# Optimization experiments

Measured on AMD Instinct MI355X. Metric: run time of the kernel, lower is better.

Reference implementation:

```python
import jax, jax.numpy as jnp
import numpy as np

L, H, P = 131072, 128, 128
STEP_RESCALE = 1.0
CONJ_SYM = True


def setup_inputs() -> dict:
    key = jax.random.key(0)
    ks = jax.random.split(key, 9)
    x = jax.random.normal(ks[0], (L, H), jnp.float32)
    # stable SSM: real parts of Lambda must be negative so |dA| < 1
    A_real_log = -(0.5 + jax.random.uniform(ks[1], (P,), jnp.float32))
    A_imag = 3.0 * jax.random.normal(ks[2], (P,), jnp.float32)
    B_re = jax.random.normal(ks[3], (P, H), jnp.float32) / np.sqrt(H)
    B_im = jax.random.normal(ks[4], (P, H), jnp.float32) / np.sqrt(H)
    C_re = jax.random.normal(ks[5], (H, P), jnp.float32) / np.sqrt(P)
    C_im = jax.random.normal(ks[6], (H, P), jnp.float32) / np.sqrt(P)
    D = jax.random.normal(ks[7], (H,), jnp.float32)
    # softplus(inv_dt) small -> small timestep dt
    inv_dt = jax.random.normal(ks[8], (P,), jnp.float32) - 4.0
    return {"x": x, "A_real_log": A_real_log, "A_imag": A_imag,
            "B_re": B_re, "B_im": B_im, "C_re": C_re, "C_im": C_im,
            "D": D, "inv_dt": inv_dt}


def reference(x, A_real_log, A_imag, B_re, B_im, C_re, C_im, D, inv_dt):
    # A = Lambda (diagonal complex state matrix), shape (P,)
    A = A_real_log + 1j * A_imag
    dt = STEP_RESCALE * jax.nn.softplus(inv_dt)            # (P,)
    # bilinear (Tustin) discretization
    BL = 1.0 / (1.0 - 0.5 * dt * A)                        # (P,)
    dA = BL * (1.0 + 0.5 * dt * A)                         # (P,)
    B = B_re + 1j * B_im                                   # (P,H)
    dB = (BL * dt)[:, None] * B                            # (P,H)
    # input projection into state space: (L,P) complex
    Bu = jnp.einsum('lh,ph->lp', x + 0j, dB)
    # linear recurrence h_k = dA * h_{k-1} + Bu_k via parallel associative scan
    A_elems = jnp.broadcast_to(dA[None, :], Bu.shape)
    def binop(q1, q2):
        a1, b1 = q1
        a2, b2 = q2
        return a1 * a2, a2 * b1 + b2
    _, hs = jax.lax.associative_scan(binop, (A_elems, Bu), axis=0)  # (L,P)
    C = C_re + 1j * C_im                                   # (H,P)
    y = jnp.einsum('lp,hp->lh', hs, C).real                # (L,H)
    if CONJ_SYM:
        y = 2.0 * y
    return y + x * D[None, :]
```

## Files before the change

### kernel.cpp

```cpp
#include <hip/hip_runtime.h>

#define L_LEN 131072
#define H_DIM 128
#define P_DIM 128
#define SEG 32
#define NSEG (L_LEN / SEG)
#define ROWS 64
#define NBLK (L_LEN / ROWS)

typedef unsigned int uint32;
typedef unsigned short u16;
typedef short bf16x8 __attribute__((ext_vector_type(8)));
typedef float f32x4 __attribute__((ext_vector_type(4)));

constexpr size_t OFF_HL  = 0;
constexpr size_t N_HLF   = (size_t)L_LEN * 256 / 2;
constexpr size_t OFF_DA  = OFF_HL + N_HLF;
constexpr size_t OFF_POW = OFF_DA + 256;
constexpr size_t OFF_E   = OFF_POW + 32 * 256;
constexpr size_t OFF_HIN = OFF_E + (size_t)NSEG * 256;
constexpr size_t OFF_W1F = OFF_HIN + (size_t)NSEG * 256;
constexpr size_t OFF_W2F = OFF_W1F + 32768;

__device__ __forceinline__ u16 f2bf(float v) {
    uint32 u = __builtin_bit_cast(uint32, v);
    uint32 r = u + 0x7FFFu + ((u >> 16) & 1u);
    return (u16)(r >> 16);
}
__device__ __forceinline__ float bf2f(u16 h) {
    uint32 u = ((uint32)h) << 16;
    return __builtin_bit_cast(float, u);
}
__device__ __forceinline__ uint32 cvtpk(float lo, float hi) {
    uint32 r;
    asm("v_cvt_pk_bf16_f32 %0, %1, %2" : "=v"(r) : "v"(lo), "v"(hi));
    return r;
}
__device__ __forceinline__ float2 cfma(float2 a, float2 h, float2 c) {
    float2 r;
    r.x = fmaf(a.x, h.x, fmaf(-a.y, h.y, c.x));
    r.y = fmaf(a.x, h.y, fmaf(a.y, h.x, c.y));
    return r;
}
__device__ __forceinline__ float2 cmul(float2 a, float2 b) {
    return make_float2(fmaf(a.x, b.x, -a.y * b.y), fmaf(a.x, b.y, a.y * b.x));
}
__device__ __forceinline__ float2 unpk(uint32 w) {
    return make_float2(bf2f((u16)(w & 0xffffu)), bf2f((u16)(w >> 16)));
}
__device__ __forceinline__ bf16x8 fixup(uint4 hl, f32x4 d0, f32x4 d1, f32x4 h0, f32x4 h1) {
    float2 c0 = cfma(make_float2(d0[0], d0[1]), make_float2(h0[0], h0[1]), unpk(hl.x));
    float2 c1 = cfma(make_float2(d0[2], d0[3]), make_float2(h0[2], h0[3]), unpk(hl.y));
    float2 c2 = cfma(make_float2(d1[0], d1[1]), make_float2(h1[0], h1[1]), unpk(hl.z));
    float2 c3 = cfma(make_float2(d1[2], d1[3]), make_float2(h1[2], h1[3]), unpk(hl.w));
    union { uint32 u[4]; bf16x8 v; } r;
    r.u[0] = cvtpk(c0.x, c0.y); r.u[1] = cvtpk(c1.x, c1.y);
    r.u[2] = cvtpk(c2.x, c2.y); r.u[3] = cvtpk(c3.x, c3.y);
    return r.v;
}

__global__ void k0(const float* __restrict__ Arl, const float* __restrict__ Ai,
                   const float* __restrict__ invdt,
                   const float* __restrict__ Bre, const float* __restrict__ Bim,
                   const float* __restrict__ Cre, const float* __restrict__ Cim,
                   float* __restrict__ dA, float* __restrict__ dApow,
                   u16* __restrict__ W1F, u16* __restrict__ W2F) {
    int tid = blockIdx.x * 256 + threadIdx.x;
    int lane = tid & 63;
    int fb = (tid >> 6) & 63;
    int ar = lane & 15, aq = lane >> 4;
    ushort4 hiA, hiB, loA, loB;
    u16* dst;
    if (tid < 4096) {
        int kt = fb >> 4, cf = fb & 15;
        int q = cf * 16 + ar;
        int p = q >> 1, c = q & 1;
        int h0 = kt * 32 + aq * 8;
        float idt = invdt[p];
        float dt = (idt > 20.f) ? idt : log1pf(expf(idt));
        float arl = Arl[p], aii = Ai[p];
        float zr = 0.5f * dt * arl, zi = 0.5f * dt * aii;
        float drr = 1.f - zr, dii = -zi;
        float inv = 1.f / (drr * drr + dii * dii);
        float blr = drr * inv, bli = -dii * inv;
        float2 s = make_float2(blr * dt, bli * dt);
        u16 hh[8], ll[8];
        #pragma unroll
        for (int j = 0; j < 8; ++j) {
            float br = Bre[p * H_DIM + h0 + j], bi = Bim[p * H_DIM + h0 + j];
            float re = fmaf(s.x, br, -s.y * bi);
            float im = fmaf(s.x, bi,  s.y * br);
            float v = c ? im : re;
            u16 h = f2bf(v); hh[j] = h; ll[j] = f2bf(v - bf2f(h));
        }
        hiA = make_ushort4(hh[0], hh[1], hh[2], hh[3]);
        hiB = make_ushort4(hh[4], hh[5], hh[6], hh[7]);
        loA = make_ushort4(ll[0], ll[1], ll[2], ll[3]);
        loB = make_ushort4(ll[4], ll[5], ll[6], ll[7]);
        dst = W1F + fb * 1024 + lane * 8;
    } else {
        int kk = fb >> 3, cf = fb & 7;
        int h = cf * 16 + ar;
        int q0 = kk * 32 + aq * 8;
        u16 hh[8], ll[8];
        #pragma unroll
        for (int j = 0; j < 8; ++j) {
            int q = q0 + j; int p = q >> 1;
            float v = (q & 1) ? (-2.f * Cim[h * P_DIM + p]) : (2.f * Cre[h * P_DIM + p]);
            u16 hv = f2bf(v); hh[j] = hv; ll[j] = f2bf(v - bf2f(hv));
        }
        hiA = make_ushort4(hh[0], hh[1], hh[2], hh[3]);
        hiB = make_ushort4(hh[4], hh[5], hh[6], hh[7]);
        loA = make_ushort4(ll[0], ll[1], ll[2], ll[3]);
        loB = make_ushort4(ll[4], ll[5], ll[6], ll[7]);
        dst = W2F + fb * 1024 + lane * 8;
    }
    *(ushort4*)(dst)       = hiA;
    *(ushort4*)(dst + 4)   = hiB;
    *(ushort4*)(dst + 512) = loA;
    *(ushort4*)(dst + 516) = loB;

    if (blockIdx.x == 0 && threadIdx.x < 128) {
        int p = threadIdx.x;
        float idt = invdt[p];
        float dt = (idt > 20.f) ? idt : log1pf(expf(idt));
        float arl = Arl[p], aii = Ai[p];
        float zr = 0.5f * dt * arl, zi = 0.5f * dt * aii;
        float drr = 1.f - zr, dii = -zi;
        float inv = 1.f / (drr * drr + dii * dii);
        float blr = drr * inv, bli = -dii * inv;
        float nr = 1.f + zr, ni = zi;
        float2 a = make_float2(fmaf(blr, nr, -bli * ni), fmaf(blr, ni, bli * nr));
        dA[2 * p] = a.x; dA[2 * p + 1] = a.y;
        float2 pw = a;
        for (int i = 0; i < SEG; ++i) {
            dApow[((size_t)i * P_DIM + p) * 2]     = pw.x;
            dApow[((size_t)i * P_DIM + p) * 2 + 1] = pw.y;
            pw = cmul(pw, a);
        }
    }
}

__global__ __launch_bounds__(256) void k1(const float* __restrict__ x,
                                          const u16* __restrict__ W1F,
                                          const float* __restrict__ dA,
                                          u16* __restrict__ HL,
                                          float* __restrict__ E) {
    __shared__ __align__(16) char smem[32768];
    u16* As_hi = (u16*)smem;
    u16* SB    = (u16*)smem;
    int t = threadIdx.x, lane = t & 63, wid = t >> 6;
    size_t l0 = (size_t)blockIdx.x * ROWS;
    int ar = lane & 15, aq = lane >> 4, ak = aq * 8;

    bf16x8 bhp[4][4];
    #pragma unroll
    for (int kt = 0; kt < 4; ++kt)
        #pragma unroll
        for (int nf = 0; nf < 4; ++nf)
            bhp[kt][nf] = *(const bf16x8*)(W1F + (size_t)(kt * 16 + wid * 4 + nf) * 1024 + lane * 8);

    float4 xv[8];
    #pragma unroll
    for (int j = 0; j < 8; ++j) {
        int f = j * 256 + t; int row = f >> 5, c4 = f & 31;
        xv[j] = *(const float4*)(x + (l0 + row) * H_DIM + c4 * 4);
    }
    #pragma unroll
    for (int j = 0; j < 8; ++j) {
        int f = j * 256 + t; int row = f >> 5, c4 = f & 31;
        uint2 wv;
        wv.x = cvtpk(xv[j].x, xv[j].y);
        wv.y = cvtpk(xv[j].z, xv[j].w);
        *(uint2*)&As_hi[row * 136 + c4 * 4] = wv;
    }
    __syncthreads();

    f32x4 acc[4][4];
    #pragma unroll
    for (int a = 0; a < 4; ++a)
        #pragma unroll
        for (int b = 0; b < 4; ++b) acc[a][b] = (f32x4)0.f;

    #pragma unroll
    for (int kt = 0; kt < 4; ++kt) {
        bf16x8 ah[4];
        #pragma unroll
        for (int mf = 0; mf < 4; ++mf) {
            int row = mf * 16 + ar;
            ah[mf] = *(const bf16x8*)&As_hi[row * 136 + kt * 32 + ak];
        }
        #pragma unroll
        for (int nf = 0; nf < 4; ++nf)
            #pragma unroll
            for (int mf = 0; mf < 4; ++mf)
                acc[mf][nf] = __builtin_amdgcn_mfma_f32_16x16x32_bf16(ah[mf], bhp[kt][nf], acc[mf][nf], 0, 0, 0);
    }
    __syncthreads();

    int sr = aq * 4;
    #pragma unroll
    for (int mf = 0; mf < 4; ++mf)
        #pragma unroll
        for (int nf = 0; nf < 4; ++nf) {
            int col = wid * 64 + nf * 16 + ar;
            uint32 w01 = cvtpk(acc[mf][nf][0], acc[mf][nf][1]);
            uint32 w23 = cvtpk(acc[mf][nf][2], acc[mf][nf][3]);
            int r0 = mf * 16 + sr;
            SB[(r0 + 0) * 256 + (((col >> 3) ^ ((r0 + 0) & 7)) << 3) + (col & 7)] = (u16)w01;
            SB[(r0 + 1) * 256 + (((col >> 3) ^ ((r0 + 1) & 7)) << 3) + (col & 7)] = (u16)(w01 >> 16);
            SB[(r0 + 2) * 256 + (((col >> 3) ^ ((r0 + 2) & 7)) << 3) + (col & 7)] = (u16)w23;
            SB[(r0 + 3) * 256 + (((col >> 3) ^ ((r0 + 3) & 7)) << 3) + (col & 7)] = (u16)(w23 >> 16);
        }
    __syncthreads();

    {
        int s = t >> 7, p = t & 127;
        float2 a = ((const float2*)dA)[p];
        uint32 buf[SEG];
        #pragma unroll
        for (int i = 0; i < SEG; ++i) {
            int row = s * 32 + i;
            buf[i] = *(const uint32*)&SB[row * 256 + (((p >> 2) ^ (row & 7)) << 3) + (p & 3) * 2];
        }
        float2 h = make_float2(0.f, 0.f);
        #pragma unroll
        for (int i = 0; i < SEG; ++i) {
            h = cfma(a, h, unpk(buf[i]));
            buf[i] = cvtpk(h.x, h.y);
        }
        #pragma unroll
        for (int i = 0; i < SEG; ++i) {
            int row = s * 32 + i;
            *(uint32*)&SB[row * 256 + (((p >> 2) ^ (row & 7)) << 3) + (p & 3) * 2] = buf[i];
        }
        ((float2*)E)[((size_t)blockIdx.x * 2 + s) * P_DIM + p] = h;
    }
    __syncthreads();

    #pragma unroll
    for (int j = 0; j < 8; ++j) {
        int f = j * 256 + t; int row = f >> 5, blk = f & 31;
        uint4 v = *(const uint4*)&SB[row * 256 + ((blk ^ (row & 7)) << 3)];
        *(uint4*)(HL + (l0 + row) * 256 + blk * 8) = v;
    }
}

__global__ __launch_bounds__(256) void k3(const float* __restrict__ E,
                                          const float* __restrict__ dA,
                                          float* __restrict__ Hin) {
    __shared__ float4 wagg[4];
    int m = blockIdx.x, t = threadIdx.x;
    int lane = t & 63, w = t >> 6;
    float2 aS = ((const float2*)dA)[m];
    #pragma unroll
    for (int i = 0; i < 5; ++i) aS = cmul(aS, aS);
    const float2* e = (const float2*)E;
    float2 ebuf[16];
    #pragma unroll
    for (int i = 0; i < 16; ++i) ebuf[i] = e[(size_t)(t * 16 + i) * P_DIM + m];
    float2 Bv = ebuf[0];
    #pragma unroll
    for (int i = 1; i < 16; ++i) Bv = cfma(aS, Bv, ebuf[i]);
    float2 Av = aS;
    #pragma unroll
    for (int i = 0; i < 4; ++i) Av = cmul(Av, Av);

    #pragma unroll
    for (int d = 1; d < 64; d <<= 1) {
        float uAx = __shfl_up(Av.x, (unsigned)d, 64);
        float uAy = __shfl_up(Av.y, (unsigned)d, 64);
        float uBx = __shfl_up(Bv.x, (unsigned)d, 64);
        float uBy = __shfl_up(Bv.y, (unsigned)d, 64);
        if (lane >= d) {
            float2 uA = make_float2(uAx, uAy), uB = make_float2(uBx, uBy);
            Bv = cfma(Av, uB, Bv);
            Av = cmul(uA, Av);
        }
    }
    if (lane == 63) wagg[w] = make_float4(Av.x, Av.y, Bv.x, Bv.y);
    __syncthreads();
    float2 Pb = make_float2(0.f, 0.f);
    for (int i = 0; i < w; ++i) {
        float4 u = wagg[i];
        float2 Wa = make_float2(u.x, u.y), Wb = make_float2(u.z, u.w);
        Pb = cfma(Wa, Pb, Wb);
    }
    float eAx = __shfl_up(Av.x, 1u, 64), eAy = __shfl_up(Av.y, 1u, 64);
    float eBx = __shfl_up(Bv.x, 1u, 64), eBy = __shfl_up(Bv.y, 1u, 64);
    float2 eA = make_float2(eAx, eAy), eB = make_float2(eBx, eBy);
    if (lane == 0) { eA = make_float2(1.f, 0.f); eB = make_float2(0.f, 0.f); }
    float2 pre = cfma(eA, Pb, eB);
    float2* hin = (float2*)Hin;
    #pragma unroll
    for (int i = 0; i < 16; ++i) {
        hin[(size_t)(t * 16 + i) * P_DIM + m] = pre;
        pre = cfma(aS, pre, ebuf[i]);
    }
}

__global__ __launch_bounds__(256) void k4(const float* __restrict__ x,
                                          const u16* __restrict__ HL,
                                          const u16* __restrict__ W2F,
                                          const float* __restrict__ dApow,
                                          const float* __restrict__ Hin,
                                          const float* __restrict__ Dv,
                                          float* __restrict__ y) {
    __shared__ __align__(16) char smem[34816];
    u16*   SB   = (u16*)smem;
    float* HinS = (float*)(smem + 32768);
    float* SBF  = (float*)smem;
    int t = threadIdx.x, lane = t & 63, wid = t >> 6;
    size_t l0 = (size_t)blockIdx.x * ROWS;

    bf16x8 bhp[8][2];
    #pragma unroll
    for (int kk = 0; kk < 8; ++kk)
        #pragma unroll
        for (int nf = 0; nf < 2; ++nf)
            bhp[kk][nf] = *(const bf16x8*)(W2F + (size_t)(kk * 8 + wid * 2 + nf) * 1024 + lane * 8);

    ((float2*)HinS)[t] = ((const float2*)Hin)[(size_t)blockIdx.x * 2 * P_DIM + t];
    __syncthreads();

    uint4 va[8];
    #pragma unroll
    for (int j = 0; j < 8; ++j) {
        int f = j * 256 + t; int row = f >> 5, blk = f & 31;
        va[j] = *(const uint4*)(HL + (l0 + row) * 256 + blk * 8);
    }
    f32x4 da[8][2];
    #pragma unroll
    for (int j = 0; j < 8; ++j) {
        int f = j * 256 + t; int row = f >> 5, blk = f & 31;
        const float* dp = dApow + (size_t)(row & 31) * 256 + blk * 8;
        da[j][0] = *(const f32x4*)dp;
        da[j][1] = *(const f32x4*)(dp + 4);
    }
    #pragma unroll
    for (int j = 0; j < 8; ++j) {
        int f = j * 256 + t; int row = f >> 5, blk = f & 31;
        int sg = row >> 5;
        f32x4 h0 = *(const f32x4*)&HinS[sg * 256 + blk * 8];
        f32x4 h1 = *(const f32x4*)&HinS[sg * 256 + blk * 8 + 4];
        bf16x8 o = fixup(va[j], da[j][0], da[j][1], h0, h1);
        *(bf16x8*)&SB[row * 256 + ((blk ^ (row & 7)) << 3)] = o;
    }
    __syncthreads();

    f32x4 acc[4][2];
    #pragma unroll
    for (int a = 0; a < 4; ++a)
        #pragma unroll
        for (int b = 0; b < 2; ++b) acc[a][b] = (f32x4)0.f;
    int ar = lane & 15, aq = lane >> 4;
    #pragma unroll
    for (int kk = 0; kk < 8; ++kk) {
        bf16x8 af[4];
        #pragma unroll
        for (int mf = 0; mf < 4; ++mf) {
            int row = mf * 16 + ar;
            int blk = kk * 4 + aq;
            af[mf] = *(const bf16x8*)&SB[row * 256 + ((blk ^ (row & 7)) << 3)];
        }
        #pragma unroll
        for (int nf = 0; nf < 2; ++nf)
            #pragma unroll
            for (int mf = 0; mf < 4; ++mf)
                acc[mf][nf] = __builtin_amdgcn_mfma_f32_16x16x32_bf16(af[mf], bhp[kk][nf], acc[mf][nf], 0, 0, 0);
    }
    __syncthreads();

    int sr = aq * 4;
    #pragma unroll
    for (int mf = 0; mf < 4; ++mf)
        #pragma unroll
        for (int nf = 0; nf < 2; ++nf)
            #pragma unroll
            for (int r = 0; r < 4; ++r) {
                int row = mf * 16 + sr + r;
                int col = wid * 32 + nf * 16 + ar;
                SBF[row * 130 + col] = acc[mf][nf][r];
            }
    __syncthreads();

    int c4 = t & 31;
    float4 dv = *(const float4*)(Dv + c4 * 4);
    #pragma unroll
    for (int j = 0; j < 8; ++j) {
        int row = j * 8 + (t >> 5);
        float4 sv = *(float4*)&SBF[row * 130 + c4 * 4];
        float4 xv = *(const float4*)(x + (l0 + row) * H_DIM + c4 * 4);
        float4 out;
        out.x = fmaf(xv.x, dv.x, sv.x);
        out.y = fmaf(xv.y, dv.y, sv.y);
        out.z = fmaf(xv.z, dv.z, sv.z);
        out.w = fmaf(xv.w, dv.w, sv.w);
        *(float4*)(y + (l0 + row) * H_DIM + c4 * 4) = out;
    }
}

extern "C" void kernel_launch(void* const* d_in, const int* in_sizes, int n_in,
                              void* d_out, int out_size, void* d_ws, size_t ws_size,
                              hipStream_t stream) {
    const float* x     = (const float*)d_in[0];
    const float* Arl   = (const float*)d_in[1];
    const float* Ai    = (const float*)d_in[2];
    const float* Bre   = (const float*)d_in[3];
    const float* Bim   = (const float*)d_in[4];
    const float* Cre   = (const float*)d_in[5];
    const float* Cim   = (const float*)d_in[6];
    const float* Dv    = (const float*)d_in[7];
    const float* invdt = (const float*)d_in[8];
    float* y  = (float*)d_out;
    float* ws = (float*)d_ws;

    u16* hl  = (u16*)(ws + OFF_HL);
    u16* w1f = (u16*)(ws + OFF_W1F);
    u16* w2f = (u16*)(ws + OFF_W2F);

    k0<<<32, 256, 0, stream>>>(Arl, Ai, invdt, Bre, Bim, Cre, Cim,
                               ws + OFF_DA, ws + OFF_POW, w1f, w2f);
    k1<<<NBLK, 256, 0, stream>>>(x, w1f, ws + OFF_DA, hl, ws + OFF_E);
    k3<<<128, 256, 0, stream>>>(ws + OFF_E, ws + OFF_DA, ws + OFF_HIN);
    k4<<<NBLK, 256, 0, stream>>>(x, hl, w2f, ws + OFF_POW,
                                 ws + OFF_HIN, Dv, y);
}
```

Measured before the change: 86.43 us.

## Recompute input projection in final kernel instead of storing local scan states

The first pass now computes only each segment's end state and no longer writes the full bf16 local hidden states (L x 256 values) to global memory. The final kernel recomputes x·dB with MFMA, runs the recurrence from the propagated carry-in state, and then applies the C projection. The dA power table and the fixup step are removed. This drops a large global write and read of the intermediate state in exchange for doing the first GEMM twice and running a serial 32-step scan in the last kernel.

```diff
diff --git a/kernel.cpp b/kernel.cpp
--- a/kernel.cpp
+++ b/kernel.cpp
@@ -13,11 +13,8 @@
 typedef short bf16x8 __attribute__((ext_vector_type(8)));
 typedef float f32x4 __attribute__((ext_vector_type(4)));
 
-constexpr size_t OFF_HL  = 0;
-constexpr size_t N_HLF   = (size_t)L_LEN * 256 / 2;
-constexpr size_t OFF_DA  = OFF_HL + N_HLF;
-constexpr size_t OFF_POW = OFF_DA + 256;
-constexpr size_t OFF_E   = OFF_POW + 32 * 256;
+constexpr size_t OFF_DA  = 0;
+constexpr size_t OFF_E   = OFF_DA + 256;
 constexpr size_t OFF_HIN = OFF_E + (size_t)NSEG * 256;
 constexpr size_t OFF_W1F = OFF_HIN + (size_t)NSEG * 256;
 constexpr size_t OFF_W2F = OFF_W1F + 32768;
@@ -48,22 +45,12 @@
 __device__ __forceinline__ float2 unpk(uint32 w) {
     return make_float2(bf2f((u16)(w & 0xffffu)), bf2f((u16)(w >> 16)));
 }
-__device__ __forceinline__ bf16x8 fixup(uint4 hl, f32x4 d0, f32x4 d1, f32x4 h0, f32x4 h1) {
-    float2 c0 = cfma(make_float2(d0[0], d0[1]), make_float2(h0[0], h0[1]), unpk(hl.x));
-    float2 c1 = cfma(make_float2(d0[2], d0[3]), make_float2(h0[2], h0[3]), unpk(hl.y));
-    float2 c2 = cfma(make_float2(d1[0], d1[1]), make_float2(h1[0], h1[1]), unpk(hl.z));
-    float2 c3 = cfma(make_float2(d1[2], d1[3]), make_float2(h1[2], h1[3]), unpk(hl.w));
-    union { uint32 u[4]; bf16x8 v; } r;
-    r.u[0] = cvtpk(c0.x, c0.y); r.u[1] = cvtpk(c1.x, c1.y);
-    r.u[2] = cvtpk(c2.x, c2.y); r.u[3] = cvtpk(c3.x, c3.y);
-    return r.v;
-}
 
 __global__ void k0(const float* __restrict__ Arl, const float* __restrict__ Ai,
                    const float* __restrict__ invdt,
                    const float* __restrict__ Bre, const float* __restrict__ Bim,
                    const float* __restrict__ Cre, const float* __restrict__ Cim,
-                   float* __restrict__ dA, float* __restrict__ dApow,
+                   float* __restrict__ dA,
                    u16* __restrict__ W1F, u16* __restrict__ W2F) {
     int tid = blockIdx.x * 256 + threadIdx.x;
     int lane = tid & 63;
@@ -130,21 +117,14 @@
         float inv = 1.f / (drr * drr + dii * dii);
         float blr = drr * inv, bli = -dii * inv;
         float nr = 1.f + zr, ni = zi;
-        float2 a = make_float2(fmaf(blr, nr, -bli * ni), fmaf(blr, ni, bli * nr));
-        dA[2 * p] = a.x; dA[2 * p + 1] = a.y;
-        float2 pw = a;
-        for (int i = 0; i < SEG; ++i) {
-            dApow[((size_t)i * P_DIM + p) * 2]     = pw.x;
-            dApow[((size_t)i * P_DIM + p) * 2 + 1] = pw.y;
-            pw = cmul(pw, a);
-        }
+        dA[2 * p]     = fmaf(blr, nr, -bli * ni);
+        dA[2 * p + 1] = fmaf(blr, ni,  bli * nr);
     }
 }
 
 __global__ __launch_bounds__(256) void k1(const float* __restrict__ x,
                                           const u16* __restrict__ W1F,
                                           const float* __restrict__ dA,
-                                          u16* __restrict__ HL,
                                           float* __restrict__ E) {
     __shared__ __align__(16) char smem[32768];
     u16* As_hi = (u16*)smem;
@@ -181,15 +161,12 @@
     for (int a = 0; a < 4; ++a)
         #pragma unroll
         for (int b = 0; b < 4; ++b) acc[a][b] = (f32x4)0.f;
-
     #pragma unroll
     for (int kt = 0; kt < 4; ++kt) {
         bf16x8 ah[4];
         #pragma unroll
-        for (int mf = 0; mf < 4; ++mf) {
-            int row = mf * 16 + ar;
-            ah[mf] = *(const bf16x8*)&As_hi[row * 136 + kt * 32 + ak];
-        }
+        for (int mf = 0; mf < 4; ++mf)
+            ah[mf] = *(const bf16x8*)&As_hi[(mf * 16 + ar) * 136 + kt * 32 + ak];
         #pragma unroll
         for (int nf = 0; nf < 4; ++nf)
             #pragma unroll
@@ -223,26 +200,10 @@
             int row = s * 32 + i;
             buf[i] = *(const uint32*)&SB[row * 256 + (((p >> 2) ^ (row & 7)) << 3) + (p & 3) * 2];
         }
-        float2 h = make_float2(0.f, 0.f);
-        #pragma unroll
-        for (int i = 0; i < SEG; ++i) {
-            h = cfma(a, h, unpk(buf[i]));
-            buf[i] = cvtpk(h.x, h.y);
-        }
-        #pragma unroll
-        for (int i = 0; i < SEG; ++i) {
-            int row = s * 32 + i;
-            *(uint32*)&SB[row * 256 + (((p >> 2) ^ (row & 7)) << 3) + (p & 3) * 2] = buf[i];
-        }
-        ((float2*)E)[((size_t)blockIdx.x * 2 + s) * P_DIM + p] = h;
-    }
-    __syncthreads();
-
-    #pragma unroll
-    for (int j = 0; j < 8; ++j) {
-        int f = j * 256 + t; int row = f >> 5, blk = f & 31;
-        uint4 v = *(const uint4*)&SB[row * 256 + ((blk ^ (row & 7)) << 3)];
-        *(uint4*)(HL + (l0 + row) * 256 + blk * 8) = v;
+        float2 e = make_float2(0.f, 0.f);
+        #pragma unroll
+        for (int i = 0; i < SEG; ++i) e = cfma(a, e, unpk(buf[i]));
+        ((float2*)E)[((size_t)blockIdx.x * 2 + s) * P_DIM + p] = e;
     }
 }
 
@@ -300,60 +261,114 @@
 }
 
 __global__ __launch_bounds__(256) void k4(const float* __restrict__ x,
-                                          const u16* __restrict__ HL,
+                                          const u16* __restrict__ W1F,
                                           const u16* __restrict__ W2F,
-                                          const float* __restrict__ dApow,
+                                          const float* __restrict__ dA,
                                           const float* __restrict__ Hin,
                                           const float* __restrict__ Dv,
                                           float* __restrict__ y) {
-    __shared__ __align__(16) char smem[34816];
-    u16*   SB   = (u16*)smem;
-    float* HinS = (float*)(smem + 32768);
-    float* SBF  = (float*)smem;
+    __shared__ __align__(16) char smem[33280];
+    u16*   As_hi = (u16*)smem;
+    u16*   SB    = (u16*)smem;
+    float* SBF   = (float*)smem;
     int t = threadIdx.x, lane = t & 63, wid = t >> 6;
     size_t l0 = (size_t)blockIdx.x * ROWS;
-
-    bf16x8 bhp[8][2];
+    int ar = lane & 15, aq = lane >> 4, ak = aq * 8;
+
+    bf16x8 bhp[4][4];
+    #pragma unroll
+    for (int kt = 0; kt < 4; ++kt)
+        #pragma unroll
+        for (int nf = 0; nf < 4; ++nf)
+            bhp[kt][nf] = *(const bf16x8*)(W1F + (size_t)(kt * 16 + wid * 4 + nf) * 1024 + lane * 8);
+
+    float4 xv[8];
+    #pragma unroll
+    for (int j = 0; j < 8; ++j) {
+        int f = j * 256 + t; int row = f >> 5, c4 = f & 31;
+        xv[j] = *(const float4*)(x + (l0 + row) * H_DIM + c4 * 4);
+    }
+    #pragma unroll
+    for (int j = 0; j < 8; ++j) {
+        int f = j * 256 + t; int row = f >> 5, c4 = f & 31;
+        uint2 wv;
+        wv.x = cvtpk(xv[j].x, xv[j].y);
+        wv.y = cvtpk(xv[j].z, xv[j].w);
+        *(uint2*)&As_hi[row * 136 + c4 * 4] = wv;
+    }
+    __syncthreads();
+
+    {
+        f32x4 acc[4][4];
+        #pragma unroll
+        for (int a = 0; a < 4; ++a)
+            #pragma unroll
+            for (int b = 0; b < 4; ++b) acc[a][b] = (f32x4)0.f;
+        #pragma unroll
+        for (int kt = 0; kt < 4; ++kt) {
+            bf16x8 ah[4];
+            #pragma unroll
+            for (int mf = 0; mf < 4; ++mf)
+                ah[mf] = *(const bf16x8*)&As_hi[(mf * 16 + ar) * 136 + kt * 32 + ak];
+            #pragma unroll
+            for (int nf = 0; nf < 4; ++nf)
+                #pragma unroll
+                for (int mf = 0; mf < 4; ++mf)
+                    acc[mf][nf] = __builtin_amdgcn_mfma_f32_16x16x32_bf16(ah[mf], bhp[kt][nf], acc[mf][nf], 0, 0, 0);
+        }
+        __syncthreads();
+        int sr = aq * 4;
+        #pragma unroll
+        for (int mf = 0; mf < 4; ++mf)
+            #pragma unroll
+            for (int nf = 0; nf < 4; ++nf) {
+                int col = wid * 64 + nf * 16 + ar;
+                uint32 w01 = cvtpk(acc[mf][nf][0], acc[mf][nf][1]);
+                uint32 w23 = cvtpk(acc[mf][nf][2], acc[mf][nf][3]);
+                int r0 = mf * 16 + sr;
+                SB[(r0 + 0) * 256 + (((col >> 3) ^ ((r0 + 0) & 7)) << 3) + (col & 7)] = (u16)w01;
+                SB[(r0 + 1) * 256 + (((col >> 3) ^ ((r0 + 1) & 7)) << 3) + (col & 7)] = (u16)(w01 >> 16);
+                SB[(r0 + 2) * 256 + (((col >> 3) ^ ((r0 + 2) & 7)) << 3) + (col & 7)] = (u16)w23;
+                SB[(r0 + 3) * 256 + (((col >> 3) ^ ((r0 + 3) & 7)) << 3) + (col & 7)] = (u16)(w23 >> 16);
+            }
+    }
+    __syncthreads();
+
+    bf16x8 bh2[8][2];
     #pragma unroll
     for (int kk = 0; kk < 8; ++kk)
         #pragma unroll
         for (int nf = 0; nf < 2; ++nf)
-            bhp[kk][nf] = *(const bf16x8*)(W2F + (size_t)(kk * 8 + wid * 2 + nf) * 1024 + lane * 8);
-
-    ((float2*)HinS)[t] = ((const float2*)Hin)[(size_t)blockIdx.x * 2 * P_DIM + t];
-    __syncthreads();
-
-    uint4 va[8];
-    #pragma unroll
-    for (int j = 0; j < 8; ++j) {
-        int f = j * 256 + t; int row = f >> 5, blk = f & 31;
-        va[j] = *(const uint4*)(HL + (l0 + row) * 256 + blk * 8);
-    }
-    f32x4 da[8][2];
-    #pragma unroll
-    for (int j = 0; j < 8; ++j) {
-        int f = j * 256 + t; int row = f >> 5, blk = f & 31;
-        const float* dp = dApow + (size_t)(row & 31) * 256 + blk * 8;
-        da[j][0] = *(const f32x4*)dp;
-        da[j][1] = *(const f32x4*)(dp + 4);
-    }
-    #pragma unroll
-    for (int j = 0; j < 8; ++j) {
-        int f = j * 256 + t; int row = f >> 5, blk = f & 31;
-        int sg = row >> 5;
-        f32x4 h0 = *(const f32x4*)&HinS[sg * 256 + blk * 8];
-        f32x4 h1 = *(const f32x4*)&HinS[sg * 256 + blk * 8 + 4];
-        bf16x8 o = fixup(va[j], da[j][0], da[j][1], h0, h1);
-        *(bf16x8*)&SB[row * 256 + ((blk ^ (row & 7)) << 3)] = o;
-    }
-    __syncthreads();
-
-    f32x4 acc[4][2];
+            bh2[kk][nf] = *(const bf16x8*)(W2F + (size_t)(kk * 8 + wid * 2 + nf) * 1024 + lane * 8);
+
+    {
+        int s = t >> 7, p = t & 127;
+        float2 a = ((const float2*)dA)[p];
+        float2 h = ((const float2*)Hin)[((size_t)blockIdx.x * 2 + s) * P_DIM + p];
+        uint32 buf[SEG];
+        #pragma unroll
+        for (int i = 0; i < SEG; ++i) {
+            int row = s * 32 + i;
+            buf[i] = *(const uint32*)&SB[row * 256 + (((p >> 2) ^ (row & 7)) << 3) + (p & 3) * 2];
+        }
+        #pragma unroll
+        for (int i = 0; i < SEG; ++i) {
+            h = cfma(a, h, unpk(buf[i]));
+            buf[i] = cvtpk(h.x, h.y);
+        }
+        #pragma unroll
+        for (int i = 0; i < SEG; ++i) {
+            int row = s * 32 + i;
+            *(uint32*)&SB[row * 256 + (((p >> 2) ^ (row & 7)) << 3) + (p & 3) * 2] = buf[i];
+        }
+    }
+    __syncthreads();
+
+    f32x4 acc2[4][2];
     #pragma unroll
     for (int a = 0; a < 4; ++a)
         #pragma unroll
-        for (int b = 0; b < 2; ++b) acc[a][b] = (f32x4)0.f;
-    int ar = lane & 15, aq = lane >> 4;
+        for (int b = 0; b < 2; ++b) acc2[a][b] = (f32x4)0.f;
     #pragma unroll
     for (int kk = 0; kk < 8; ++kk) {
         bf16x8 af[4];
@@ -367,7 +382,7 @@
         for (int nf = 0; nf < 2; ++nf)
             #pragma unroll
             for (int mf = 0; mf < 4; ++mf)
-                acc[mf][nf] = __builtin_amdgcn_mfma_f32_16x16x32_bf16(af[mf], bhp[kk][nf], acc[mf][nf], 0, 0, 0);
+                acc2[mf][nf] = __builtin_amdgcn_mfma_f32_16x16x32_bf16(af[mf], bh2[kk][nf], acc2[mf][nf], 0, 0, 0);
     }
     __syncthreads();
 
@@ -380,7 +395,7 @@
             for (int r = 0; r < 4; ++r) {
                 int row = mf * 16 + sr + r;
                 int col = wid * 32 + nf * 16 + ar;
-                SBF[row * 130 + col] = acc[mf][nf][r];
+                SBF[row * 130 + col] = acc2[mf][nf][r];
             }
     __syncthreads();
 
@@ -390,12 +405,12 @@
     for (int j = 0; j < 8; ++j) {
         int row = j * 8 + (t >> 5);
         float4 sv = *(float4*)&SBF[row * 130 + c4 * 4];
-        float4 xv = *(const float4*)(x + (l0 + row) * H_DIM + c4 * 4);
+        float4 xr = *(const float4*)(x + (l0 + row) * H_DIM + c4 * 4);
         float4 out;
-        out.x = fmaf(xv.x, dv.x, sv.x);
-        out.y = fmaf(xv.y, dv.y, sv.y);
-        out.z = fmaf(xv.z, dv.z, sv.z);
-        out.w = fmaf(xv.w, dv.w, sv.w);
+        out.x = fmaf(xr.x, dv.x, sv.x);
+        out.y = fmaf(xr.y, dv.y, sv.y);
+        out.z = fmaf(xr.z, dv.z, sv.z);
+        out.w = fmaf(xr.w, dv.w, sv.w);
         *(float4*)(y + (l0 + row) * H_DIM + c4 * 4) = out;
     }
 }
@@ -415,14 +430,13 @@
     float* y  = (float*)d_out;
     float* ws = (float*)d_ws;
 
-    u16* hl  = (u16*)(ws + OFF_HL);
     u16* w1f = (u16*)(ws + OFF_W1F);
     u16* w2f = (u16*)(ws + OFF_W2F);
 
     k0<<<32, 256, 0, stream>>>(Arl, Ai, invdt, Bre, Bim, Cre, Cim,
-                               ws + OFF_DA, ws + OFF_POW, w1f, w2f);
-    k1<<<NBLK, 256, 0, stream>>>(x, w1f, ws + OFF_DA, hl, ws + OFF_E);
+                               ws + OFF_DA, w1f, w2f);
+    k1<<<NBLK, 256, 0, stream>>>(x, w1f, ws + OFF_DA, ws + OFF_E);
     k3<<<128, 256, 0, stream>>>(ws + OFF_E, ws + OFF_DA, ws + OFF_HIN);
-    k4<<<NBLK, 256, 0, stream>>>(x, hl, w2f, ws + OFF_POW,
+    k4<<<NBLK, 256, 0, stream>>>(x, w1f, w2f, ws + OFF_DA,
                                  ws + OFF_HIN, Dv, y);
 }
```

Result: faster. 82.27 us (-4.8%).
